# Optimization experiments

Measured on AMD Instinct MI355X. Metric: run time of the kernel, lower is better.

## Reference

```python
import jax, jax.numpy as jnp
import numpy as np

B, S, DM = 4, 2048, 1024
H, D, R = 16, 64, 8

def setup_inputs() -> dict:
    key = jax.random.key(0)
    ks = jax.random.split(key, 32)
    def rn(k, shape, scale=0.02):
        return jax.random.normal(k, shape, dtype=jnp.float32) * scale
    inp = {
        'queries': jax.random.normal(ks[0], (B, S, DM), dtype=jnp.float32),
        'keys':    jax.random.normal(ks[1], (B, S, DM), dtype=jnp.float32),
        'values':  jax.random.normal(ks[2], (B, S, DM), dtype=jnp.float32),
        # base projections, stored [in, out]
        'Wq_w': rn(ks[3], (DM, H * D)), 'Wq_b': jnp.zeros((H * D,), jnp.float32),
        'Wk_w': rn(ks[4], (DM, H * D)), 'Wk_b': jnp.zeros((H * D,), jnp.float32),
        'Wv_w': rn(ks[5], (DM, H * D)), 'Wv_b': jnp.zeros((H * D,), jnp.float32),
        # LoRA adapters (A: in->rank, B: rank->out), Linear layers so both have biases
        'Aq_w': rn(ks[6], (DM, R)), 'Aq_b': jnp.zeros((R,), jnp.float32),
        'Bq_w': rn(ks[7], (R, H * D)), 'Bq_b': jnp.zeros((H * D,), jnp.float32),
        'Ak_w': rn(ks[8], (DM, R)), 'Ak_b': jnp.zeros((R,), jnp.float32),
        'Bk_w': rn(ks[9], (R, H * D)), 'Bk_b': jnp.zeros((H * D,), jnp.float32),
        'Av_w': rn(ks[10], (DM, R)), 'Av_b': jnp.zeros((R,), jnp.float32),
        'Bv_w': rn(ks[11], (R, H * D)), 'Bv_b': jnp.zeros((H * D,), jnp.float32),
        # output merge
        'Wo_w': rn(ks[12], (H * D, DM)), 'Wo_b': jnp.zeros((DM,), jnp.float32),
    }
    return inp


def _attn(queries, keys, values, Wq_w, Wq_b, Wk_w, Wk_b, Wv_w, Wv_b,
          Aq_w, Aq_b, Bq_w, Bq_b, Ak_w, Ak_b, Bk_w, Bk_b, Av_w, Av_b, Bv_w, Bv_b,
          Wo_w, Wo_b):
    b, s, _ = queries.shape
    # QKV projections fused with LoRA low-rank additions
    q = queries @ Wq_w + Wq_b + ((queries @ Aq_w + Aq_b) @ Bq_w + Bq_b)
    k = keys    @ Wk_w + Wk_b + ((keys    @ Ak_w + Ak_b) @ Bk_w + Bk_b)
    # NOTE: source applies the V LoRA adapter to `keys` (self.Av(keys)) - replicated
    v = values  @ Wv_w + Wv_b + ((keys    @ Av_w + Av_b) @ Bv_w + Bv_b)
    q = q.reshape(b, s, H, D).transpose(0, 2, 1, 3)  # [B,H,S,D]
    k = k.reshape(b, s, H, D).transpose(0, 2, 1, 3)
    v = v.reshape(b, s, H, D).transpose(0, 2, 1, 3)
    att = jnp.einsum('bhqd,bhkd->bhqk', q, k)        # [B,H,Sq,Sk]
    causal = jnp.tril(jnp.ones((s, s), dtype=bool))
    att = jnp.where(causal, att, -jnp.inf)
    # NOTE: source softmaxes over dim=2 (query axis) and scales AFTER softmax
    att = jax.nn.softmax(att, axis=2) / jnp.sqrt(jnp.asarray(D, att.dtype))
    out = jnp.einsum('bhqk,bhkd->bhqd', att, v)      # [B,H,S,D]
    out = out.transpose(0, 2, 1, 3).reshape(b, s, H * D)
    return out @ Wo_w + Wo_b


def reference(queries, keys, values, Wq_w, Wq_b, Wk_w, Wk_b, Wv_w, Wv_b,
              Aq_w, Aq_b, Bq_w, Bq_b, Ak_w, Ak_b, Bk_w, Bk_b, Av_w, Av_b, Bv_w, Bv_b,
              Wo_w, Wo_b):
    return _attn(queries, keys, values, Wq_w, Wq_b, Wk_w, Wk_b, Wv_w, Wv_b,
                 Aq_w, Aq_b, Bq_w, Bq_b, Ak_w, Ak_b, Bk_w, Bk_b, Av_w, Av_b, Bv_w, Bv_b,
                 Wo_w, Wo_b)
```

## Files before the change

### kernel.cpp

```cpp
#include <hip/hip_runtime.h>
#include <math.h>
#include <stdint.h>

typedef __bf16 bf16;
typedef __bf16 bf16x8 __attribute__((ext_vector_type(8)));
typedef __bf16 bf16x4 __attribute__((ext_vector_type(4)));
typedef float  floatx4 __attribute__((ext_vector_type(4)));

#define MFMA16(a, b, c) __builtin_amdgcn_mfma_f32_16x16x32_bf16(a, b, c, 0, 0, 0)
#define EXP2(x) __builtin_amdgcn_exp2f(x)

static constexpr int S  = 2048;
static constexpr int DM = 1024;
static constexpr int Dh = 64;
#define NEGBIG (-1e30f)
#define LOG2E  1.44269504088896340736f

__device__ __forceinline__ void gload16(const void* g, void* l) {
  __builtin_amdgcn_global_load_lds(
      (const __attribute__((address_space(1))) void*)(uintptr_t)g,
      (__attribute__((address_space(3))) void*)(uintptr_t)l,
      16, 0, 0);
}

__global__ __launch_bounds__(256) void prep_convert(
    const float* __restrict__ q, const float* __restrict__ k,
    const float* __restrict__ v, bf16* __restrict__ X)
{
  int s = blockIdx.x;
  int c = threadIdx.x * 4;
  size_t src = (size_t)s * DM + c;
  float4 qv = *(const float4*)(q + src);
  float4 vv = *(const float4*)(v + src);
  float4 kv = *(const float4*)(k + src);
  size_t dst = (size_t)s * (3 * DM);
  bf16x4 t;
  t[0] = (bf16)qv.x; t[1] = (bf16)qv.y; t[2] = (bf16)qv.z; t[3] = (bf16)qv.w;
  *(bf16x4*)(X + dst + c) = t;
  t[0] = (bf16)vv.x; t[1] = (bf16)vv.y; t[2] = (bf16)vv.z; t[3] = (bf16)vv.w;
  *(bf16x4*)(X + dst + DM + c) = t;
  t[0] = (bf16)kv.x; t[1] = (bf16)kv.y; t[2] = (bf16)kv.z; t[3] = (bf16)kv.w;
  *(bf16x4*)(X + dst + 2 * DM + c) = t;
}

__global__ __launch_bounds__(256) void fold_weights(
    const float* __restrict__ Wq, const float* __restrict__ Aq, const float* __restrict__ Bq,
    const float* __restrict__ Wk, const float* __restrict__ Ak, const float* __restrict__ Bk,
    const float* __restrict__ Wv, const float* __restrict__ Av, const float* __restrict__ Bv,
    const float* __restrict__ Wo,
    bf16* __restrict__ WqT, bf16* __restrict__ WkT,
    bf16* __restrict__ WvT, bf16* __restrict__ WoT)
{
  __shared__ float tile[32][33];
  const int tx = threadIdx.x, ty = threadIdx.y;
  const int n0 = blockIdx.x * 32, k0 = blockIdx.y * 32;
  for (int mi = 0; mi < 5; ++mi) {
    #pragma unroll
    for (int i = 0; i < 4; ++i) {
      int k = k0 + ty + i * 8, n = n0 + tx;
      float val = 0.f;
      if (mi == 0) {
        val = Wq[(size_t)k * DM + n];
        #pragma unroll
        for (int r = 0; r < 8; ++r) val += Aq[k * 8 + r] * Bq[(size_t)r * DM + n];
      } else if (mi == 1) {
        val = Wk[(size_t)k * DM + n];
        #pragma unroll
        for (int r = 0; r < 8; ++r) val += Ak[k * 8 + r] * Bk[(size_t)r * DM + n];
      } else if (mi == 2) {
        val = Wv[(size_t)k * DM + n];
      } else if (mi == 3) {
        #pragma unroll
        for (int r = 0; r < 8; ++r) val += Av[k * 8 + r] * Bv[(size_t)r * DM + n];
      } else {
        val = Wo[(size_t)k * DM + n];
      }
      tile[ty + i * 8][tx] = val;
    }
    __syncthreads();
    #pragma unroll
    for (int i = 0; i < 4; ++i) {
      int n = n0 + ty + i * 8, k = k0 + tx;
      float val = tile[tx][ty + i * 8];
      if (mi == 0)      WqT[(size_t)n * DM + k] = (bf16)val;
      else if (mi == 1) WkT[(size_t)n * DM + k] = (bf16)val;
      else if (mi == 2) WvT[(size_t)n * 2048 + k] = (bf16)val;
      else if (mi == 3) WvT[(size_t)n * 2048 + 1024 + k] = (bf16)val;
      else              WoT[(size_t)n * DM + k] = (bf16)val;
    }
    __syncthreads();
  }
}

__global__ __launch_bounds__(256) void fold_bias(
    const float* __restrict__ Wqb, const float* __restrict__ Aqb,
    const float* __restrict__ BqW, const float* __restrict__ Bqb,
    const float* __restrict__ Wkb, const float* __restrict__ Akb,
    const float* __restrict__ BkW, const float* __restrict__ Bkb,
    const float* __restrict__ Wvb, const float* __restrict__ Avb,
    const float* __restrict__ BvW, const float* __restrict__ Bvb,
    const float* __restrict__ Wob,
    float* __restrict__ bq, float* __restrict__ bk,
    float* __restrict__ bv, float* __restrict__ bo)
{
  int n = blockIdx.x * 256 + threadIdx.x;
  float aq = Wqb[n] + Bqb[n];
  float ak = Wkb[n] + Bkb[n];
  float av = Wvb[n] + Bvb[n];
  #pragma unroll
  for (int r = 0; r < 8; ++r) {
    aq += Aqb[r] * BqW[(size_t)r * DM + n];
    ak += Akb[r] * BkW[(size_t)r * DM + n];
    av += Avb[r] * BvW[(size_t)r * DM + n];
  }
  bq[n] = aq; bk[n] = ak; bv[n] = av; bo[n] = Wob[n];
}

__global__ __launch_bounds__(256) void gemm_bf16(
    const bf16* __restrict__ A, int lda,
    const bf16* __restrict__ BT, int ldb,
    const float* __restrict__ bias,
    int M, int N, int K, float oscale,
    float* __restrict__ outF, bf16* __restrict__ outB, int mode)
{
  __shared__ bf16 sA[128 * 32];
  __shared__ bf16 sB[128 * 32];
  const int tid = threadIdx.x;
  const int bm0 = blockIdx.y * 128, bn0 = blockIdx.x * 128;
  const int w = tid >> 6, lane = tid & 63, lrow = lane & 15, quad = lane >> 4;
  const int wm = (w >> 1) * 64, wn = (w & 1) * 64;

  const int srow = lane >> 2;
  const int scol = (lane & 3) * 8;
  const bf16* Ag0 = A  + (size_t)(bm0 + w * 32 + srow) * lda + scol;
  const bf16* Ag1 = A  + (size_t)(bm0 + w * 32 + 16 + srow) * lda + scol;
  const bf16* Bg0 = BT + (size_t)(bn0 + w * 32 + srow) * ldb + scol;
  const bf16* Bg1 = BT + (size_t)(bn0 + w * 32 + 16 + srow) * ldb + scol;
  bf16* sA0 = &sA[(w * 32) * 32];
  bf16* sA1 = &sA[(w * 32 + 16) * 32];
  bf16* sB0 = &sB[(w * 32) * 32];
  bf16* sB1 = &sB[(w * 32 + 16) * 32];

  floatx4 zero = {0.f, 0.f, 0.f, 0.f};
  floatx4 acc[4][4];
  #pragma unroll
  for (int i = 0; i < 4; ++i)
    #pragma unroll
    for (int j = 0; j < 4; ++j) acc[i][j] = zero;

  for (int kt = 0; kt < K; kt += 32) {
    __syncthreads();
    gload16(Ag0 + kt, sA0);
    gload16(Ag1 + kt, sA1);
    gload16(Bg0 + kt, sB0);
    gload16(Bg1 + kt, sB1);
    __syncthreads();
    bf16x8 aF[4], bF[4];
    #pragma unroll
    for (int i = 0; i < 4; ++i)
      aF[i] = *(const bf16x8*)&sA[(wm + i * 16 + lrow) * 32 + quad * 8];
    #pragma unroll
    for (int j = 0; j < 4; ++j)
      bF[j] = *(const bf16x8*)&sB[(wn + j * 16 + lrow) * 32 + quad * 8];
    #pragma unroll
    for (int i = 0; i < 4; ++i)
      #pragma unroll
      for (int j = 0; j < 4; ++j)
        acc[i][j] = MFMA16(aF[i], bF[j], acc[i][j]);
  }

  if (mode == 3) {
    #pragma unroll
    for (int i = 0; i < 4; ++i) {
      #pragma unroll
      for (int r = 0; r < 4; ++r) {
        int gm = bm0 + wm + i * 16 + quad * 4 + r;
        float bvr = bias[gm];
        int h = gm >> 6, d = gm & 63;
        #pragma unroll
        for (int j = 0; j < 4; ++j) {
          int gn = bn0 + wn + j * 16 + lrow;
          int b = gn >> 11, s = gn & 2047;
          outB[((size_t)(b * 16 + h) * 64 + d) * 2048 + s] =
              (bf16)(acc[i][j][r] + bvr);
        }
      }
    }
    return;
  }

  float bvs[4];
  #pragma unroll
  for (int j = 0; j < 4; ++j) bvs[j] = bias[bn0 + wn + j * 16 + lrow];

  #pragma unroll
  for (int i = 0; i < 4; ++i) {
    #pragma unroll
    for (int j = 0; j < 4; ++j) {
      #pragma unroll
      for (int r = 0; r < 4; ++r) {
        int gm = bm0 + wm + i * 16 + quad * 4 + r;
        int gn = bn0 + wn + j * 16 + lrow;
        float v = (acc[i][j][r] + bvs[j]) * oscale;
        if (mode == 0) {
          outF[(size_t)gm * N + gn] = v;
        } else {
          int b = gm >> 11, s = gm & 2047, h = gn >> 6, d = gn & 63;
          outB[((size_t)(b * 16 + h) * 2048 + s) * 64 + d] = (bf16)v;
        }
      }
    }
  }
}

__global__ __launch_bounds__(256) void attn_pass1(
    const bf16* __restrict__ Qb, const bf16* __restrict__ Kb,
    float* __restrict__ statC)
{
  const int bh = blockIdx.y;
  const int x = blockIdx.x;
  const int q0a = x * 64, q0b = (31 - x) * 64;
  const int tid = threadIdx.x;
  const int w = tid >> 6, lane = tid & 63, lrow = lane & 15, quad = lane >> 4;
  const bf16* Qh = Qb + (size_t)bh * S * Dh;
  const bf16* Kh = Kb + (size_t)bh * S * Dh;

  int cbase[8];
  #pragma unroll
  for (int cf = 0; cf < 8; ++cf)
    cbase[cf] = (cf < 4) ? (q0a + cf * 16) : (q0b + (cf - 4) * 16);

  bf16x8 kf[8][2];
  #pragma unroll
  for (int cf = 0; cf < 8; ++cf) {
    const bf16* kp = Kh + (size_t)(cbase[cf] + lrow) * Dh + quad * 8;
    kf[cf][0] = *(const bf16x8*)kp;
    kf[cf][1] = *(const bf16x8*)(kp + 32);
  }

  float rm[8], rs[8];
  #pragma unroll
  for (int cf = 0; cf < 8; ++cf) { rm[cf] = NEGBIG; rs[cf] = 0.f; }

  const int qs = q0a + w * 16;
  const bf16* qp0 = Qh + (size_t)(qs + lrow) * Dh + quad * 8;
  bf16x8 a0 = *(const bf16x8*)qp0, a1 = *(const bf16x8*)(qp0 + 32);

  for (int q0 = qs; q0 < S; q0 += 64) {
    bf16x8 n0 = a0, n1 = a1;
    if (q0 + 64 < S) {
      const bf16* np = Qh + (size_t)(q0 + 64 + lrow) * Dh + quad * 8;
      n0 = *(const bf16x8*)np; n1 = *(const bf16x8*)(np + 32);
    }
    #pragma unroll
    for (int cf = 0; cf < 8; ++cf) {
      const int c0f = cbase[cf];
      if (c0f > q0 + 15) continue;
      floatx4 sacc = {0.f, 0.f, 0.f, 0.f};
      sacc = MFMA16(a0, kf[cf][0], sacc);
      sacc = MFMA16(a1, kf[cf][1], sacc);
      float v0 = sacc[0], v1 = sacc[1], v2 = sacc[2], v3 = sacc[3];
      if (q0 < c0f + 15) {
        int c = c0f + lrow, qb = q0 + quad * 4;
        v0 = (qb + 0 >= c) ? v0 : NEGBIG;
        v1 = (qb + 1 >= c) ? v1 : NEGBIG;
        v2 = (qb + 2 >= c) ? v2 : NEGBIG;
        v3 = (qb + 3 >= c) ? v3 : NEGBIG;
      }
      float mt = fmaxf(fmaxf(v0, v1), fmaxf(v2, v3));
      float nm = fmaxf(rm[cf], mt);
      rs[cf] = rs[cf] * EXP2(rm[cf] - nm)
             + EXP2(v0 - nm) + EXP2(v1 - nm)
             + EXP2(v2 - nm) + EXP2(v3 - nm);
      rm[cf] = nm;
    }
    a0 = n0; a1 = n1;
  }

  #pragma unroll
  for (int cf = 0; cf < 8; ++cf) {
    #pragma unroll
    for (int off = 16; off < 64; off <<= 1) {
      float om = __shfl_xor(rm[cf], off, 64);
      float os = __shfl_xor(rs[cf], off, 64);
      float nm = fmaxf(rm[cf], om);
      rs[cf] = rs[cf] * EXP2(rm[cf] - nm) + os * EXP2(om - nm);
      rm[cf] = nm;
    }
  }

  __shared__ float smm[4][128];
  __shared__ float sms[4][128];
  if (quad == 0) {
    #pragma unroll
    for (int cf = 0; cf < 8; ++cf) {
      smm[w][cf * 16 + lrow] = rm[cf];
      sms[w][cf * 16 + lrow] = rs[cf];
    }
  }
  __syncthreads();
  if (tid < 128) {
    float m = smm[0][tid], sum = sms[0][tid];
    #pragma unroll
    for (int ww = 1; ww < 4; ++ww) {
      float om = smm[ww][tid], os = sms[ww][tid];
      float nm = fmaxf(m, om);
      sum = sum * EXP2(m - nm) + os * EXP2(om - nm);
      m = nm;
    }
    int col = (tid < 64) ? (q0a + tid) : (q0b + tid - 64);
    statC[(size_t)bh * S + col] = m + 3.0f + __log2f(sum);
  }
}

__global__ __launch_bounds__(256) void attn_pass2(
    const bf16* __restrict__ Qb, const bf16* __restrict__ Kb,
    const bf16* __restrict__ Vt, const float* __restrict__ statC,
    bf16* __restrict__ AttOut)
{
  const int bh = blockIdx.y;
  const int x = blockIdx.x;
  const int q0a = x * 64, q0b = (31 - x) * 64;
  const int tid = threadIdx.x;
  const int w = tid >> 6, lane = tid & 63, lrow = lane & 15, quad = lane >> 4;
  const bf16* Qh = Qb + (size_t)bh * S * Dh;
  const bf16* Kh = Kb + (size_t)bh * S * Dh;
  const bf16* Vh = Vt + (size_t)bh * Dh * S;
  const float* sth = statC + (size_t)bh * S;

  __shared__ bf16 sK[64][9][8];
  __shared__ bf16 sV[64][9][8];
  __shared__ bf16 pbuf[4][32][9][8];

  const int r0m[2] = { q0a + w * 16, q0b + w * 16 };
  bf16x8 qf[2][2];
  #pragma unroll
  for (int mi = 0; mi < 2; ++mi) {
    const bf16* qp = Qh + (size_t)(r0m[mi] + lrow) * Dh + quad * 8;
    qf[mi][0] = *(const bf16x8*)qp;
    qf[mi][1] = *(const bf16x8*)(qp + 32);
  }

  floatx4 zero = {0.f, 0.f, 0.f, 0.f};
  floatx4 accO[2][4];
  #pragma unroll
  for (int mi = 0; mi < 2; ++mi)
    #pragma unroll
    for (int nf = 0; nf < 4; ++nf) accO[mi][nf] = zero;

  const int sr = tid >> 3;
  const int g  = tid & 7;
  const int nT = 32 - x;
  bf16* const pw = &pbuf[w][0][0][0];

  bf16x8 kg0 = *(const bf16x8*)(Kh + (size_t)sr * Dh + g * 8);
  bf16x8 kg1 = *(const bf16x8*)(Kh + (size_t)(sr + 32) * Dh + g * 8);
  bf16x8 vg0 = *(const bf16x8*)(Vh + (size_t)sr * S + g * 8);
  bf16x8 vg1 = *(const bf16x8*)(Vh + (size_t)(sr + 32) * S + g * 8);
  float  creg = sth[lane];

  for (int kt = 0; kt < nT; ++kt) {
    const int kc = kt * 64;
    __syncthreads();
    *(bf16x8*)&sK[sr][g][0]      = kg0;
    *(bf16x8*)&sK[sr + 32][g][0] = kg1;
    *(bf16x8*)&sV[sr][g][0]      = vg0;
    *(bf16x8*)&sV[sr + 32][g][0] = vg1;
    const float ccur = creg;
    __syncthreads();
    if (kt + 1 < nT) {
      const int kn = kc + 64;
      kg0 = *(const bf16x8*)(Kh + (size_t)(kn + sr) * Dh + g * 8);
      kg1 = *(const bf16x8*)(Kh + (size_t)(kn + sr + 32) * Dh + g * 8);
      vg0 = *(const bf16x8*)(Vh + (size_t)sr * S + kn + g * 8);
      vg1 = *(const bf16x8*)(Vh + (size_t)(sr + 32) * S + kn + g * 8);
      creg = sth[kn + lane];
    }

    bool actH[2][2];
    #pragma unroll
    for (int mi = 0; mi < 2; ++mi) {
      actH[mi][0] = kc      <= r0m[mi] + 15;
      actH[mi][1] = kc + 32 <= r0m[mi] + 15;
    }

    #pragma unroll
    for (int cf = 0; cf < 4; ++cf) {
      const int hh = cf >> 1;
      if (!actH[0][hh] && !actH[1][hh]) continue;
      const int c0f = kc + cf * 16;
      const int cl = cf * 16;
      bf16x8 kf0 = *(const bf16x8*)&sK[cl + lrow][quad][0];
      bf16x8 kf1 = *(const bf16x8*)&sK[cl + lrow][4 + quad][0];
      float Cc = __shfl(ccur, cf * 16 + lrow, 64);
      const int c = c0f + lrow;
      #pragma unroll
      for (int mi = 0; mi < 2; ++mi) {
        if (!actH[mi][hh]) continue;
        const int r0 = r0m[mi];
        const int prow = mi * 16 + quad * 4;
        if (c0f > r0 + 15) {
          #pragma unroll
          for (int r = 0; r < 4; ++r)
            pw[(prow + r) * 72 + cf * 16 + lrow] = (bf16)0.f;
        } else {
          floatx4 sacc = zero;
          sacc = MFMA16(qf[mi][0], kf0, sacc);
          sacc = MFMA16(qf[mi][1], kf1, sacc);
          const bool fullf = (c0f + 15 <= r0);
          #pragma unroll
          for (int r = 0; r < 4; ++r) {
            float p = EXP2(sacc[r] - Cc);
            if (!fullf) p = (c <= r0 + quad * 4 + r) ? p : 0.f;
            pw[(prow + r) * 72 + cf * 16 + lrow] = (bf16)p;
          }
        }
      }
    }

    #pragma unroll
    for (int hh = 0; hh < 2; ++hh) {
      if (!actH[0][hh] && !actH[1][hh]) continue;
      bf16x8 vf[4];
      #pragma unroll
      for (int nf = 0; nf < 4; ++nf)
        vf[nf] = *(const bf16x8*)&sV[nf * 16 + lrow][hh * 4 + quad][0];
      #pragma unroll
      for (int mi = 0; mi < 2; ++mi) {
        if (!actH[mi][hh]) continue;
        bf16x8 pf = *(const bf16x8*)&pbuf[w][mi * 16 + lrow][hh * 4 + quad][0];
        #pragma unroll
        for (int nf = 0; nf < 4; ++nf)
          accO[mi][nf] = MFMA16(pf, vf[nf], accO[mi][nf]);
      }
    }
  }

  const int b = bh >> 4, h = bh & 15;
  #pragma unroll
  for (int mi = 0; mi < 2; ++mi) {
    #pragma unroll
    for (int nf = 0; nf < 4; ++nf) {
      #pragma unroll
      for (int r = 0; r < 4; ++r) {
        int qq = r0m[mi] + quad * 4 + r;
        int d = nf * 16 + lrow;
        AttOut[((size_t)(b * S + qq)) * DM + h * 64 + d] = (bf16)accO[mi][nf][r];
      }
    }
  }
}

extern "C" void kernel_launch(void* const* d_in, const int* in_sizes, int n_in,
                              void* d_out, int out_size, void* d_ws, size_t ws_size,
                              hipStream_t stream) {
  (void)in_sizes; (void)n_in; (void)out_size; (void)ws_size;
  const float* queries = (const float*)d_in[0];
  const float* keys    = (const float*)d_in[1];
  const float* values  = (const float*)d_in[2];
  const float* Wq_w = (const float*)d_in[3];  const float* Wq_b = (const float*)d_in[4];
  const float* Wk_w = (const float*)d_in[5];  const float* Wk_b = (const float*)d_in[6];
  const float* Wv_w = (const float*)d_in[7];  const float* Wv_b = (const float*)d_in[8];
  const float* Aq_w = (const float*)d_in[9];  const float* Aq_b = (const float*)d_in[10];
  const float* Bq_w = (const float*)d_in[11]; const float* Bq_b = (const float*)d_in[12];
  const float* Ak_w = (const float*)d_in[13]; const float* Ak_b = (const float*)d_in[14];
  const float* Bk_w = (const float*)d_in[15]; const float* Bk_b = (const float*)d_in[16];
  const float* Av_w = (const float*)d_in[17]; const float* Av_b = (const float*)d_in[18];
  const float* Bv_w = (const float*)d_in[19]; const float* Bv_b = (const float*)d_in[20];
  const float* Wo_w = (const float*)d_in[21]; const float* Wo_b = (const float*)d_in[22];
  float* out = (float*)d_out;

  char* ws = (char*)d_ws;
  size_t off = 0;
  auto alloc = [&](size_t bytes) -> void* {
    void* p = ws + off;
    off += (bytes + 255) & ~(size_t)255;
    return p;
  };
  bf16*  X_all  = (bf16*)alloc((size_t)8192 * 3072 * 2);
  bf16*  Qb     = (bf16*)alloc((size_t)64 * 2048 * 64 * 2);
  bf16*  Kb     = (bf16*)alloc((size_t)64 * 2048 * 64 * 2);
  bf16*  Vt     = (bf16*)alloc((size_t)64 * 64 * 2048 * 2);
  bf16*  AttOut = (bf16*)alloc((size_t)8192 * 1024 * 2);
  bf16*  WqT    = (bf16*)alloc((size_t)1024 * 1024 * 2);
  bf16*  WkT    = (bf16*)alloc((size_t)1024 * 1024 * 2);
  bf16*  WvT    = (bf16*)alloc((size_t)1024 * 2048 * 2);
  bf16*  WoT    = (bf16*)alloc((size_t)1024 * 1024 * 2);
  float* bq     = (float*)alloc(1024 * 4);
  float* bk     = (float*)alloc(1024 * 4);
  float* bv     = (float*)alloc(1024 * 4);
  float* bo     = (float*)alloc(1024 * 4);
  float* statC  = (float*)alloc((size_t)64 * 2048 * 4);

  prep_convert<<<8192, 256, 0, stream>>>(queries, keys, values, X_all);
  fold_weights<<<dim3(32, 32), dim3(32, 8), 0, stream>>>(
      Wq_w, Aq_w, Bq_w, Wk_w, Ak_w, Bk_w, Wv_w, Av_w, Bv_w, Wo_w,
      WqT, WkT, WvT, WoT);
  fold_bias<<<4, 256, 0, stream>>>(
      Wq_b, Aq_b, Bq_w, Bq_b, Wk_b, Ak_b, Bk_w, Bk_b,
      Wv_b, Av_b, Bv_w, Bv_b, Wo_b, bq, bk, bv, bo);

  gemm_bf16<<<dim3(8, 64), 256, 0, stream>>>(X_all,        3072, WqT, 1024, bq, 8192, 1024, 1024, LOG2E, nullptr, Qb, 1);
  gemm_bf16<<<dim3(8, 64), 256, 0, stream>>>(X_all + 2048, 3072, WkT, 1024, bk, 8192, 1024, 1024, 1.0f,  nullptr, Kb, 1);
  gemm_bf16<<<dim3(64, 8), 256, 0, stream>>>(WvT, 2048, X_all + 1024, 3072, bv, 1024, 8192, 2048, 1.0f, nullptr, Vt, 3);

  attn_pass1<<<dim3(16, 64), 256, 0, stream>>>(Qb, Kb, statC);
  attn_pass2<<<dim3(16, 64), 256, 0, stream>>>(Qb, Kb, Vt, statC, AttOut);

  gemm_bf16<<<dim3(8, 64), 256, 0, stream>>>(AttOut, 1024, WoT, 1024, bo, 8192, 1024, 1024, 1.0f, out, nullptr, 0);
}
```

Baseline: 480.3 us.

## Swizzle attention LDS tiles and transpose score MFMA for vectorized P stores

```diff
diff --git a/kernel.cpp b/kernel.cpp
--- a/kernel.cpp
+++ b/kernel.cpp
@@ -21,6 +21,10 @@
       (const __attribute__((address_space(1))) void*)(uintptr_t)g,
       (__attribute__((address_space(3))) void*)(uintptr_t)l,
       16, 0, 0);
+}
+
+__device__ __forceinline__ int swz(int row, int g) {
+  return row * 64 + ((g ^ (row & 7)) << 3);
 }
 
 __global__ __launch_bounds__(256) void prep_convert(
@@ -328,9 +332,9 @@
   const bf16* Vh = Vt + (size_t)bh * Dh * S;
   const float* sth = statC + (size_t)bh * S;
 
-  __shared__ bf16 sK[64][9][8];
-  __shared__ bf16 sV[64][9][8];
-  __shared__ bf16 pbuf[4][32][9][8];
+  __shared__ bf16 sK[64 * 64];
+  __shared__ bf16 sV[64 * 64];
+  __shared__ bf16 pbuf[4][32 * 64];
 
   const int r0m[2] = { q0a + w * 16, q0b + w * 16 };
   bf16x8 qf[2][2];
@@ -351,22 +355,24 @@
   const int sr = tid >> 3;
   const int g  = tid & 7;
   const int nT = 32 - x;
-  bf16* const pw = &pbuf[w][0][0][0];
+  bf16* const pw = &pbuf[w][0];
 
   bf16x8 kg0 = *(const bf16x8*)(Kh + (size_t)sr * Dh + g * 8);
   bf16x8 kg1 = *(const bf16x8*)(Kh + (size_t)(sr + 32) * Dh + g * 8);
   bf16x8 vg0 = *(const bf16x8*)(Vh + (size_t)sr * S + g * 8);
   bf16x8 vg1 = *(const bf16x8*)(Vh + (size_t)(sr + 32) * S + g * 8);
-  float  creg = sth[lane];
 
   for (int kt = 0; kt < nT; ++kt) {
     const int kc = kt * 64;
     __syncthreads();
-    *(bf16x8*)&sK[sr][g][0]      = kg0;
-    *(bf16x8*)&sK[sr + 32][g][0] = kg1;
-    *(bf16x8*)&sV[sr][g][0]      = vg0;
-    *(bf16x8*)&sV[sr + 32][g][0] = vg1;
-    const float ccur = creg;
+    *(bf16x8*)&sK[swz(sr, g)]      = kg0;
+    *(bf16x8*)&sK[swz(sr + 32, g)] = kg1;
+    *(bf16x8*)&sV[swz(sr, g)]      = vg0;
+    *(bf16x8*)&sV[swz(sr + 32, g)] = vg1;
+    float4 c4[4];
+    #pragma unroll
+    for (int cf = 0; cf < 4; ++cf)
+      c4[cf] = *(const float4*)&sth[kc + cf * 16 + quad * 4];
     __syncthreads();
     if (kt + 1 < nT) {
       const int kn = kc + 64;
@@ -374,7 +380,6 @@
       kg1 = *(const bf16x8*)(Kh + (size_t)(kn + sr + 32) * Dh + g * 8);
       vg0 = *(const bf16x8*)(Vh + (size_t)sr * S + kn + g * 8);
       vg1 = *(const bf16x8*)(Vh + (size_t)(sr + 32) * S + kn + g * 8);
-      creg = sth[kn + lane];
     }
 
     bool actH[2][2];
@@ -390,31 +395,34 @@
       if (!actH[0][hh] && !actH[1][hh]) continue;
       const int c0f = kc + cf * 16;
       const int cl = cf * 16;
-      bf16x8 kf0 = *(const bf16x8*)&sK[cl + lrow][quad][0];
-      bf16x8 kf1 = *(const bf16x8*)&sK[cl + lrow][4 + quad][0];
-      float Cc = __shfl(ccur, cf * 16 + lrow, 64);
-      const int c = c0f + lrow;
+      bf16x8 kf0 = *(const bf16x8*)&sK[swz(cl + lrow, quad)];
+      bf16x8 kf1 = *(const bf16x8*)&sK[swz(cl + lrow, 4 + quad)];
+      const float* cc = &c4[cf].x;
+      const int crb = c0f + quad * 4;
       #pragma unroll
       for (int mi = 0; mi < 2; ++mi) {
         if (!actH[mi][hh]) continue;
         const int r0 = r0m[mi];
-        const int prow = mi * 16 + quad * 4;
+        const int gq = cf * 2 + (quad >> 1);
+        const int poff = (mi * 16 + lrow) * 64 +
+                         ((gq ^ (lrow & 7)) << 3) + (quad & 1) * 4;
+        bf16x4 pk;
         if (c0f > r0 + 15) {
-          #pragma unroll
-          for (int r = 0; r < 4; ++r)
-            pw[(prow + r) * 72 + cf * 16 + lrow] = (bf16)0.f;
+          pk[0] = pk[1] = pk[2] = pk[3] = (bf16)0.f;
         } else {
           floatx4 sacc = zero;
-          sacc = MFMA16(qf[mi][0], kf0, sacc);
-          sacc = MFMA16(qf[mi][1], kf1, sacc);
+          sacc = MFMA16(kf0, qf[mi][0], sacc);
+          sacc = MFMA16(kf1, qf[mi][1], sacc);
           const bool fullf = (c0f + 15 <= r0);
+          const int qlane = r0 + lrow;
           #pragma unroll
           for (int r = 0; r < 4; ++r) {
-            float p = EXP2(sacc[r] - Cc);
-            if (!fullf) p = (c <= r0 + quad * 4 + r) ? p : 0.f;
-            pw[(prow + r) * 72 + cf * 16 + lrow] = (bf16)p;
+            float p = EXP2(sacc[r] - cc[r]);
+            if (!fullf) p = (crb + r <= qlane) ? p : 0.f;
+            pk[r] = (bf16)p;
           }
         }
+        *(bf16x4*)(pw + poff) = pk;
       }
     }
 
@@ -424,11 +432,11 @@
       bf16x8 vf[4];
       #pragma unroll
       for (int nf = 0; nf < 4; ++nf)
-        vf[nf] = *(const bf16x8*)&sV[nf * 16 + lrow][hh * 4 + quad][0];
+        vf[nf] = *(const bf16x8*)&sV[swz(nf * 16 + lrow, hh * 4 + quad)];
       #pragma unroll
       for (int mi = 0; mi < 2; ++mi) {
         if (!actH[mi][hh]) continue;
-        bf16x8 pf = *(const bf16x8*)&pbuf[w][mi * 16 + lrow][hh * 4 + quad][0];
+        bf16x8 pf = *(const bf16x8*)(pw + swz(mi * 16 + lrow, hh * 4 + quad));
         #pragma unroll
         for (int nf = 0; nf < 4; ++nf)
           accO[mi][nf] = MFMA16(pf, vf[nf], accO[mi][nf]);
```

Measured after the change: 474.3 us. About the same (-1.2%).
